# Performance work log

Hardware: AMD Instinct MI355X
Metric: run time of the kernel (lower is better)

## Reference

```python
import jax, jax.numpy as jnp
import numpy as np

D_ENC = 512
D_DEC = 512
JOINT = 512
VOCAB = 1024


def setup_inputs() -> dict:
    key = jax.random.key(0)
    ks = jax.random.split(key, 7)
    B, T, U = 4, 256, 64
    s_enc = 1.0 / np.sqrt(D_ENC)
    s_dec = 1.0 / np.sqrt(D_DEC)
    s_out = 1.0 / np.sqrt(JOINT)
    return {
        "encoder_out": jax.random.normal(ks[0], (B, T, 1, D_ENC), dtype=jnp.float32),
        "decoder_out": jax.random.normal(ks[1], (B, 1, U, D_DEC), dtype=jnp.float32),
        # torch.nn.Linear stores weight as (out, in); uniform(-1/sqrt(in), 1/sqrt(in))
        "W_enc": jax.random.uniform(ks[2], (JOINT, D_ENC), jnp.float32, -s_enc, s_enc),
        "b_enc": jax.random.uniform(ks[3], (JOINT,), jnp.float32, -s_enc, s_enc),
        "W_dec": jax.random.uniform(ks[4], (JOINT, D_DEC), jnp.float32, -s_dec, s_dec),
        "W_out": jax.random.uniform(ks[5], (VOCAB, JOINT), jnp.float32, -s_out, s_out),
        "b_out": jax.random.uniform(ks[6], (VOCAB,), jnp.float32, -s_out, s_out),
    }


def reference(encoder_out, decoder_out, W_enc, b_enc, W_dec, W_out, b_out):
    # Project each side in its small shape first (B,T,1,J) and (B,1,U,J),
    # then broadcast-add over (T,U), tanh, output GEMM -> (B,T,U,V).
    enc = jnp.einsum("btud,jd->btuj", encoder_out, W_enc) + b_enc  # (B,T,1,J)
    dec = jnp.einsum("btud,jd->btuj", decoder_out, W_dec)          # (B,1,U,J)
    h = jnp.tanh(enc + dec)                                        # (B,T,U,J)
    return jnp.einsum("btuj,vj->btuv", h, W_out) + b_out           # (B,T,U,V)
```

## Files before the change

kernel.cpp:

```cpp
#include <hip/hip_runtime.h>
#include <hip/hip_bf16.h>


typedef __attribute__((ext_vector_type(8))) short short8;
typedef __attribute__((ext_vector_type(4))) float f32x4;
typedef __attribute__((ext_vector_type(16))) float f32x16;

#define SZ0 524288
#define SZ1 131072
#define SZ2 262144
#define SZ3 512
#define SZ4 262144
#define SZ5 524288
#define SZ6 1024
#define CU0 0
#define CU1 524288
#define CU2 655360
#define CU3 917504
#define CU4 918016
#define CU5 1180160
#define CU6 1704448
#define CTOT 1705472

__global__ void detect_kernel(const void* p0, const void* p1, const void* p2,
                              const void* p3, const void* p4, const void* p5,
                              const void* p6, int* flags) {
  const void* ps[7] = {p0, p1, p2, p3, p4, p5, p6};
  const int sz[7] = {SZ0, SZ1, SZ2, SZ3, SZ4, SZ5, SZ6};
  const int w = threadIdx.x >> 6;
  const int l = threadIdx.x & 63;
  if (w >= 7) return;
  const unsigned short* u = (const unsigned short*)ps[w];
  const int lim = sz[w] < 1024 ? sz[w] : 1024;
  int bad = 0;
  for (int j = l; j < lim; j += 64) {
    const unsigned e = (u[j] >> 7) & 0xFFu;
    if (e >= 0x8Eu) bad = 1;
  }
  const unsigned long long b = __ballot(bad);
  if (l == 0) flags[w] = (b != 0ULL) ? 1 : 0;
}

__global__ __launch_bounds__(256) void convert_kernel(
    const void* p0, const void* p1, const void* p2, const void* p3,
    const void* p4, const void* p5, const void* p6,
    const int* __restrict__ flags, __hip_bfloat16* __restrict__ dst) {
  const int gid = blockIdx.x * 256 + threadIdx.x;
  if (gid >= CTOT) return;
  int t, local;
  const void* p;
  if (gid < CU1)      { t = 0; local = gid - CU0; p = p0; }
  else if (gid < CU2) { t = 1; local = gid - CU1; p = p1; }
  else if (gid < CU3) { t = 2; local = gid - CU2; p = p2; }
  else if (gid < CU4) { t = 3; local = gid - CU3; p = p3; }
  else if (gid < CU5) { t = 4; local = gid - CU4; p = p4; }
  else if (gid < CU6) { t = 5; local = gid - CU5; p = p5; }
  else                { t = 6; local = gid - CU6; p = p6; }
  __hip_bfloat16 v;
  if (flags[t])
    v = __float2bfloat16(((const float*)p)[local]);
  else
    v = ((const __hip_bfloat16*)p)[local];
  dst[gid] = v;
}

__device__ __forceinline__ void gemm_bt_body(
    const __hip_bfloat16* __restrict__ A, const __hip_bfloat16* __restrict__ Bw,
    const __hip_bfloat16* __restrict__ bias, float* __restrict__ C,
    int M, int N, int K, int bid,
    __hip_bfloat16* sA, __hip_bfloat16* sB) {
  const int tid = threadIdx.x;
  const int w = tid >> 6;
  const int l = tid & 63;
  const int ntiles = N >> 7;
  const int mt = bid / ntiles;
  const int nt = bid % ntiles;
  const int m0 = mt << 7;
  const int n0 = nt << 7;
  const int wm = (w >> 1) << 6;
  const int wn = (w & 1) << 6;
  const int r16 = l & 15;
  const int q = l >> 4;

  f32x4 acc[4][4] = {};

  const int srow_in = l >> 3;
  const int scol = (l & 7) << 3;

  for (int k0 = 0; k0 < K; k0 += 64) {
#pragma unroll
    for (int i = 0; i < 4; ++i) {
      const int c = (w << 2) + i;
      const int row = (c << 3) + srow_in;
      const __hip_bfloat16* gA = A + (size_t)(m0 + row) * K + k0 + scol;
      const __hip_bfloat16* gB = Bw + (size_t)(n0 + row) * K + k0 + scol;
      __builtin_amdgcn_global_load_lds(
          (const __attribute__((address_space(1))) void*)gA,
          (__attribute__((address_space(3))) void*)(sA + (c << 9) + (l << 3)),
          16, 0, 0);
      __builtin_amdgcn_global_load_lds(
          (const __attribute__((address_space(1))) void*)gB,
          (__attribute__((address_space(3))) void*)(sB + (c << 9) + (l << 3)),
          16, 0, 0);
    }
    __syncthreads();

#pragma unroll
    for (int kk = 0; kk < 2; ++kk) {
      const int kc = (kk << 5) + (q << 3);
      short8 af[4], bf[4];
#pragma unroll
      for (int mi = 0; mi < 4; ++mi)
        af[mi] = *(const short8*)(sA + (wm + (mi << 4) + r16) * 64 + kc);
#pragma unroll
      for (int ni = 0; ni < 4; ++ni)
        bf[ni] = *(const short8*)(sB + (wn + (ni << 4) + r16) * 64 + kc);
#pragma unroll
      for (int mi = 0; mi < 4; ++mi)
#pragma unroll
        for (int ni = 0; ni < 4; ++ni)
          acc[mi][ni] = __builtin_amdgcn_mfma_f32_16x16x32_bf16(
              af[mi], bf[ni], acc[mi][ni], 0, 0, 0);
    }
    __syncthreads();
  }

#pragma unroll
  for (int ni = 0; ni < 4; ++ni) {
    const int col = n0 + wn + (ni << 4) + r16;
    const float bc = bias ? __bfloat162float(bias[col]) : 0.0f;
#pragma unroll
    for (int mi = 0; mi < 4; ++mi) {
      const int rowb = m0 + wm + (mi << 4) + (q << 2);
#pragma unroll
      for (int i = 0; i < 4; ++i)
        C[(size_t)(rowb + i) * N + col] = acc[mi][ni][i] + bc;
    }
  }
}

__global__ __launch_bounds__(256) void proj_kernel(
    const __hip_bfloat16* __restrict__ enc, const __hip_bfloat16* __restrict__ Wenc,
    const __hip_bfloat16* __restrict__ benc,
    const __hip_bfloat16* __restrict__ dec, const __hip_bfloat16* __restrict__ Wdec,
    float* __restrict__ Pe, float* __restrict__ Pd) {
  __shared__ __align__(16) __hip_bfloat16 sA[128 * 64];
  __shared__ __align__(16) __hip_bfloat16 sB[128 * 64];
  if (blockIdx.x < 32)
    gemm_bt_body(enc, Wenc, benc, Pe, 1024, 512, 512, blockIdx.x, sA, sB);
  else
    gemm_bt_body(dec, Wdec, nullptr, Pd, 256, 512, 512, blockIdx.x - 32, sA, sB);
}

__global__ __launch_bounds__(512, 2) void gemm_joint(
    const float* __restrict__ Pe, const float* __restrict__ Pd,
    const __hip_bfloat16* __restrict__ Bw,
    const __hip_bfloat16* __restrict__ bias, float* __restrict__ out) {
  __shared__ __align__(16) __hip_bfloat16 sH[64 * 512];
  __shared__ __align__(16) __hip_bfloat16 sB[2 * 16384];

  const int t = threadIdx.x;
  const int w = t >> 6;
  const int l = t & 63;
  const int l31 = l & 31;
  const int q2 = l >> 5;
  const int m0 = blockIdx.x << 6;

  auto stage = [&](int ks, int bufbit) {
#pragma unroll
    for (int h = 0; h < 4; ++h) {
      const int n = (w << 7) + (h << 5) + (l >> 1);
      const __hip_bfloat16* src =
          Bw + (size_t)n * 512 + (ks << 4) + ((l & 1) << 3);
      __builtin_amdgcn_global_load_lds(
          (const __attribute__((address_space(1))) void*)src,
          (__attribute__((address_space(3))) void*)(
              sB + (bufbit << 14) + ((((w << 2) + h) << 9) + (l << 3))),
          16, 0, 0);
    }
  };

  stage(0, 0);

  {
    const int r = l;
    const int seg = w;
    const int d = ((blockIdx.x >> 8) << 6) | r;
    const float* pe = Pe + (size_t)blockIdx.x * 512 + (seg << 6);
    const float* pd = Pd + (size_t)d * 512 + (seg << 6);
#pragma unroll
    for (int i = 0; i < 8; ++i) {
      const int cc = (seg << 3) + i;
      const f32x4 a0 = *(const f32x4*)(pe + (i << 3));
      const f32x4 a1 = *(const f32x4*)(pe + (i << 3) + 4);
      const f32x4 b0 = *(const f32x4*)(pd + (i << 3));
      const f32x4 b1 = *(const f32x4*)(pd + (i << 3) + 4);
      short8 hv;
#pragma unroll
      for (int jj = 0; jj < 4; ++jj) {
        float s = a0[jj] + b0[jj];
        float tv = 1.0f - 2.0f / (__expf(2.0f * s) + 1.0f);
        __hip_bfloat16 hb = __float2bfloat16(tv);
        hv[jj] = *(const short*)&hb;
        s = a1[jj] + b1[jj];
        tv = 1.0f - 2.0f / (__expf(2.0f * s) + 1.0f);
        hb = __float2bfloat16(tv);
        hv[4 + jj] = *(const short*)&hb;
      }
      *(short8*)(sH + (r << 9) + ((cc ^ r) << 3)) = hv;
    }
  }
  __syncthreads();

  const int wn = w << 7;
  f32x16 acc[2][4] = {};

  for (int ks = 0; ks < 32; ++ks) {
    const int bufbit = ks & 1;
    if (ks < 31) {
      stage(ks + 1, bufbit ^ 1);
      asm volatile("s_waitcnt vmcnt(4)" ::: "memory");
    } else {
      asm volatile("s_waitcnt vmcnt(0)" ::: "memory");
    }
    __builtin_amdgcn_sched_barrier(0);
    __builtin_amdgcn_s_barrier();
    __builtin_amdgcn_sched_barrier(0);

    const int cb = (ks << 1) + q2;
    short8 af[2];
#pragma unroll
    for (int mi = 0; mi < 2; ++mi) {
      const int r = (mi << 5) + l31;
      af[mi] = *(const short8*)(sH + (r << 9) + ((cb ^ r) << 3));
    }
    short8 bf[4];
#pragma unroll
    for (int ni = 0; ni < 4; ++ni)
      bf[ni] = *(const short8*)(sB + (bufbit << 14) +
                                ((wn + (ni << 5) + l31) << 4) + (q2 << 3));
#pragma unroll
    for (int mi = 0; mi < 2; ++mi)
#pragma unroll
      for (int ni = 0; ni < 4; ++ni)
        acc[mi][ni] = __builtin_amdgcn_mfma_f32_32x32x16_bf16(
            af[mi], bf[ni], acc[mi][ni], 0, 0, 0);

    __builtin_amdgcn_sched_barrier(0);
    __builtin_amdgcn_s_barrier();
    __builtin_amdgcn_sched_barrier(0);
  }

#pragma unroll
  for (int ni = 0; ni < 4; ++ni) {
    const int col = wn + (ni << 5) + l31;
    const float bc = __bfloat162float(bias[col]);
#pragma unroll
    for (int mi = 0; mi < 2; ++mi) {
#pragma unroll
      for (int rr = 0; rr < 16; ++rr) {
        const int row = m0 + (mi << 5) + (rr & 3) + ((rr >> 2) << 3) + (q2 << 2);
        out[(size_t)row * 1024 + col] = acc[mi][ni][rr] + bc;
      }
    }
  }
}

extern "C" void kernel_launch(void* const* d_in, const int* in_sizes, int n_in,
                              void* d_out, int out_size, void* d_ws,
                              size_t ws_size, hipStream_t stream) {
  char* ws = (char*)d_ws;
  int* flags = (int*)ws;
  __hip_bfloat16* cp = (__hip_bfloat16*)(ws + 256);
  float* Pe = (float*)(ws + (4ull << 20));
  float* Pd = (float*)(ws + (6ull << 20));

  detect_kernel<<<dim3(1), dim3(512), 0, stream>>>(
      d_in[0], d_in[1], d_in[2], d_in[3], d_in[4], d_in[5], d_in[6], flags);
  convert_kernel<<<dim3((CTOT + 255) / 256), dim3(256), 0, stream>>>(
      d_in[0], d_in[1], d_in[2], d_in[3], d_in[4], d_in[5], d_in[6], flags, cp);

  const __hip_bfloat16* enc_c = cp + CU0;
  const __hip_bfloat16* dec_c = cp + CU1;
  const __hip_bfloat16* Wenc_c = cp + CU2;
  const __hip_bfloat16* benc_c = cp + CU3;
  const __hip_bfloat16* Wdec_c = cp + CU4;
  const __hip_bfloat16* Wout_c = cp + CU5;
  const __hip_bfloat16* bout_c = cp + CU6;

  proj_kernel<<<dim3(40), dim3(256), 0, stream>>>(enc_c, Wenc_c, benc_c,
                                                  dec_c, Wdec_c, Pe, Pd);
  gemm_joint<<<dim3(1024), dim3(512), 0, stream>>>(
      Pe, Pd, Wout_c, bout_c, (float*)d_out);
}
```

Measured before the change: 472.9 us.

## Retile joint GEMM to 128x256 blocks and compute tanh activations in-register

The joint GEMM changes from 64-row blocks covering all 1024 output columns to 128x256 tiles, doubling the grid. The tanh(enc+dec) activation tile is no longer staged in shared memory. Each warp reads Pe/Pd straight from global memory per k-step and builds its MFMA A fragments in registers, using a hardware reciprocal in place of a division. B tiles are 64-wide in k, XOR-swizzled, and double-buffered, and the reduced LDS allows a 4-blocks-per-CU occupancy hint. The cost is that tanh is recomputed for each of the 4 column blocks and the fp32 Pe/Pd reads from global move into the inner loop.

Result: faster. 445.5 us (-5.8%).

```diff
diff --git a/kernel.cpp b/kernel.cpp
--- a/kernel.cpp
+++ b/kernel.cpp
@@ -4,6 +4,7 @@
 
 typedef __attribute__((ext_vector_type(8))) short short8;
 typedef __attribute__((ext_vector_type(4))) float f32x4;
+typedef __attribute__((ext_vector_type(8))) float f32x8;
 typedef __attribute__((ext_vector_type(16))) float f32x16;
 
 #define SZ0 524288
@@ -152,73 +153,53 @@
     gemm_bt_body(dec, Wdec, nullptr, Pd, 256, 512, 512, blockIdx.x - 32, sA, sB);
 }
 
-__global__ __launch_bounds__(512, 2) void gemm_joint(
+__global__ __launch_bounds__(512, 4) void gemm_joint(
     const float* __restrict__ Pe, const float* __restrict__ Pd,
     const __hip_bfloat16* __restrict__ Bw,
     const __hip_bfloat16* __restrict__ bias, float* __restrict__ out) {
-  __shared__ __align__(16) __hip_bfloat16 sH[64 * 512];
-  __shared__ __align__(16) __hip_bfloat16 sB[2 * 16384];
+  __shared__ __align__(16) __hip_bfloat16 sB[2][256 * 64];
 
   const int t = threadIdx.x;
   const int w = t >> 6;
   const int l = t & 63;
   const int l31 = l & 31;
   const int q2 = l >> 5;
-  const int m0 = blockIdx.x << 6;
-
-  auto stage = [&](int ks, int bufbit) {
+  const int mb = blockIdx.x >> 2;
+  const int nb = blockIdx.x & 3;
+  const int m0 = mb << 7;
+  const int n0 = nb << 8;
+
+  auto stage = [&](int kt, int b) {
+    const int r_ = t >> 3;
+    const int c_ = t & 7;
 #pragma unroll
     for (int h = 0; h < 4; ++h) {
-      const int n = (w << 7) + (h << 5) + (l >> 1);
+      const int r = (h << 6) + r_;
       const __hip_bfloat16* src =
-          Bw + (size_t)n * 512 + (ks << 4) + ((l & 1) << 3);
+          Bw + (size_t)(n0 + r) * 512 + (kt << 6) + ((c_ ^ (r & 7)) << 3);
       __builtin_amdgcn_global_load_lds(
           (const __attribute__((address_space(1))) void*)src,
           (__attribute__((address_space(3))) void*)(
-              sB + (bufbit << 14) + ((((w << 2) + h) << 9) + (l << 3))),
+              &sB[b][0] + (h << 12) + (t << 3)),
           16, 0, 0);
     }
   };
 
+  const int wm = (w >> 1) << 5;
+  const int wn = (w & 1) << 7;
+
+  const float* peRow = Pe + (size_t)((m0 + wm) >> 6) * 512;
+  const int d = (((m0 >> 14) << 6) | ((wm + l31) & 63));
+  const float* pdRow = Pd + (size_t)d * 512;
+
+  f32x16 acc[4] = {};
+
   stage(0, 0);
 
-  {
-    const int r = l;
-    const int seg = w;
-    const int d = ((blockIdx.x >> 8) << 6) | r;
-    const float* pe = Pe + (size_t)blockIdx.x * 512 + (seg << 6);
-    const float* pd = Pd + (size_t)d * 512 + (seg << 6);
-#pragma unroll
-    for (int i = 0; i < 8; ++i) {
-      const int cc = (seg << 3) + i;
-      const f32x4 a0 = *(const f32x4*)(pe + (i << 3));
-      const f32x4 a1 = *(const f32x4*)(pe + (i << 3) + 4);
-      const f32x4 b0 = *(const f32x4*)(pd + (i << 3));
-      const f32x4 b1 = *(const f32x4*)(pd + (i << 3) + 4);
-      short8 hv;
-#pragma unroll
-      for (int jj = 0; jj < 4; ++jj) {
-        float s = a0[jj] + b0[jj];
-        float tv = 1.0f - 2.0f / (__expf(2.0f * s) + 1.0f);
-        __hip_bfloat16 hb = __float2bfloat16(tv);
-        hv[jj] = *(const short*)&hb;
-        s = a1[jj] + b1[jj];
-        tv = 1.0f - 2.0f / (__expf(2.0f * s) + 1.0f);
-        hb = __float2bfloat16(tv);
-        hv[4 + jj] = *(const short*)&hb;
-      }
-      *(short8*)(sH + (r << 9) + ((cc ^ r) << 3)) = hv;
-    }
-  }
-  __syncthreads();
-
-  const int wn = w << 7;
-  f32x16 acc[2][4] = {};
-
-  for (int ks = 0; ks < 32; ++ks) {
-    const int bufbit = ks & 1;
-    if (ks < 31) {
-      stage(ks + 1, bufbit ^ 1);
+  for (int kt = 0; kt < 8; ++kt) {
+    const int b = kt & 1;
+    if (kt < 7) {
+      stage(kt + 1, b ^ 1);
       asm volatile("s_waitcnt vmcnt(4)" ::: "memory");
     } else {
       asm volatile("s_waitcnt vmcnt(0)" ::: "memory");
@@ -227,24 +208,33 @@
     __builtin_amdgcn_s_barrier();
     __builtin_amdgcn_sched_barrier(0);
 
-    const int cb = (ks << 1) + q2;
-    short8 af[2];
-#pragma unroll
-    for (int mi = 0; mi < 2; ++mi) {
-      const int r = (mi << 5) + l31;
-      af[mi] = *(const short8*)(sH + (r << 9) + ((cb ^ r) << 3));
-    }
-    short8 bf[4];
-#pragma unroll
-    for (int ni = 0; ni < 4; ++ni)
-      bf[ni] = *(const short8*)(sB + (bufbit << 14) +
-                                ((wn + (ni << 5) + l31) << 4) + (q2 << 3));
-#pragma unroll
-    for (int mi = 0; mi < 2; ++mi)
+#pragma unroll
+    for (int j = 0; j < 4; ++j) {
+      const int kk = (kt << 6) + (j << 4) + (q2 << 3);
+      const f32x8 pe8 = *(const f32x8*)(peRow + kk);
+      const f32x8 pd8 = *(const f32x8*)(pdRow + kk);
+      short8 af;
+#pragma unroll
+      for (int x = 0; x < 8; ++x) {
+        const float s = pe8[x] + pd8[x];
+        const float u = __expf(2.0f * s);
+        const float tv = 1.0f - 2.0f * __builtin_amdgcn_rcpf(u + 1.0f);
+        const __hip_bfloat16 hb = __float2bfloat16(tv);
+        af[x] = *(const short*)&hb;
+      }
+      const int c = (j << 1) + q2;
+      short8 bf[4];
+#pragma unroll
+      for (int ni = 0; ni < 4; ++ni) {
+        const int row = wn + (ni << 5) + l31;
+        bf[ni] = *(const short8*)(&sB[b][0] + (row << 6) +
+                                  ((c ^ (row & 7)) << 3));
+      }
 #pragma unroll
       for (int ni = 0; ni < 4; ++ni)
-        acc[mi][ni] = __builtin_amdgcn_mfma_f32_32x32x16_bf16(
-            af[mi], bf[ni], acc[mi][ni], 0, 0, 0);
+        acc[ni] = __builtin_amdgcn_mfma_f32_32x32x16_bf16(
+            af, bf[ni], acc[ni], 0, 0, 0);
+    }
 
     __builtin_amdgcn_sched_barrier(0);
     __builtin_amdgcn_s_barrier();
@@ -253,15 +243,12 @@
 
 #pragma unroll
   for (int ni = 0; ni < 4; ++ni) {
-    const int col = wn + (ni << 5) + l31;
+    const int col = n0 + wn + (ni << 5) + l31;
     const float bc = __bfloat162float(bias[col]);
 #pragma unroll
-    for (int mi = 0; mi < 2; ++mi) {
-#pragma unroll
-      for (int rr = 0; rr < 16; ++rr) {
-        const int row = m0 + (mi << 5) + (rr & 3) + ((rr >> 2) << 3) + (q2 << 2);
-        out[(size_t)row * 1024 + col] = acc[mi][ni][rr] + bc;
-      }
+    for (int rr = 0; rr < 16; ++rr) {
+      const int row = m0 + wm + (rr & 3) + ((rr >> 2) << 3) + (q2 << 2);
+      out[(size_t)row * 1024 + col] = acc[ni][rr] + bc;
     }
   }
 }
@@ -290,6 +277,6 @@
 
   proj_kernel<<<dim3(40), dim3(256), 0, stream>>>(enc_c, Wenc_c, benc_c,
                                                   dec_c, Wdec_c, Pe, Pd);
-  gemm_joint<<<dim3(1024), dim3(512), 0, stream>>>(
+  gemm_joint<<<dim3(2048), dim3(512), 0, stream>>>(
       Pe, Pd, Wout_c, bout_c, (float*)d_out);
 }
```

## Pre-transpose W_out into k-chunk layout and stream H tile in quarters

Applied to the files above, without the earlier changes.

Extra blocks in the projection kernel write a copy of W_out reordered into k-chunk-major layout, so each stage of the joint GEMM loads one contiguous 32 KB slab with fully coalesced global_load_lds. The joint kernel now builds the tanh H tile in four 128-column quarters instead of all 512 columns at once. This shrinks the H LDS buffer from 64 KB to 16 KB, which may allow more resident blocks. The price is an extra syncthreads and a global reload of Pe/Pd every 8 k-steps, an added transpose pass over W_out, and an rcp-based tanh in place of a division.

New measurement: 423.4 us. -10.5%, faster.

```diff
diff --git a/kernel.cpp b/kernel.cpp
--- a/kernel.cpp
+++ b/kernel.cpp
@@ -4,6 +4,7 @@
 
 typedef __attribute__((ext_vector_type(8))) short short8;
 typedef __attribute__((ext_vector_type(4))) float f32x4;
+typedef __attribute__((ext_vector_type(8))) float f32x8;
 typedef __attribute__((ext_vector_type(16))) float f32x16;
 
 #define SZ0 524288
@@ -143,21 +144,33 @@
     const __hip_bfloat16* __restrict__ enc, const __hip_bfloat16* __restrict__ Wenc,
     const __hip_bfloat16* __restrict__ benc,
     const __hip_bfloat16* __restrict__ dec, const __hip_bfloat16* __restrict__ Wdec,
+    const __hip_bfloat16* __restrict__ Wout, __hip_bfloat16* __restrict__ WT,
     float* __restrict__ Pe, float* __restrict__ Pd) {
   __shared__ __align__(16) __hip_bfloat16 sA[128 * 64];
   __shared__ __align__(16) __hip_bfloat16 sB[128 * 64];
-  if (blockIdx.x < 32)
+  if (blockIdx.x < 32) {
     gemm_bt_body(enc, Wenc, benc, Pe, 1024, 512, 512, blockIdx.x, sA, sB);
-  else
+  } else if (blockIdx.x < 40) {
     gemm_bt_body(dec, Wdec, nullptr, Pd, 256, 512, 512, blockIdx.x - 32, sA, sB);
+  } else {
+    const int bid = blockIdx.x - 40;
+#pragma unroll
+    for (int i = 0; i < 32; ++i) {
+      const int cid = (bid << 13) + (i << 8) + threadIdx.x;
+      const int n = cid >> 6;
+      const int c = cid & 63;
+      *(short8*)(WT + (((size_t)c << 10) + n) * 8) =
+          *(const short8*)(Wout + (size_t)n * 512 + (c << 3));
+    }
+  }
 }
 
 __global__ __launch_bounds__(512, 2) void gemm_joint(
     const float* __restrict__ Pe, const float* __restrict__ Pd,
-    const __hip_bfloat16* __restrict__ Bw,
+    const __hip_bfloat16* __restrict__ WT,
     const __hip_bfloat16* __restrict__ bias, float* __restrict__ out) {
-  __shared__ __align__(16) __hip_bfloat16 sH[64 * 512];
-  __shared__ __align__(16) __hip_bfloat16 sB[2 * 16384];
+  __shared__ __align__(16) __hip_bfloat16 sH[16 * 64 * 8];
+  __shared__ __align__(16) __hip_bfloat16 sB[2][2 * 1024 * 8];
 
   const int t = threadIdx.x;
   const int w = t >> 6;
@@ -165,60 +178,54 @@
   const int l31 = l & 31;
   const int q2 = l >> 5;
   const int m0 = blockIdx.x << 6;
-
-  auto stage = [&](int ks, int bufbit) {
+  const int wn = w << 7;
+
+  auto stage = [&](int ks, int b) {
+    const __hip_bfloat16* src = WT + ((size_t)ks << 14);
 #pragma unroll
     for (int h = 0; h < 4; ++h) {
-      const int n = (w << 7) + (h << 5) + (l >> 1);
-      const __hip_bfloat16* src =
-          Bw + (size_t)n * 512 + (ks << 4) + ((l & 1) << 3);
+      const int slot = (h << 9) + t;
       __builtin_amdgcn_global_load_lds(
-          (const __attribute__((address_space(1))) void*)src,
-          (__attribute__((address_space(3))) void*)(
-              sB + (bufbit << 14) + ((((w << 2) + h) << 9) + (l << 3))),
+          (const __attribute__((address_space(1))) void*)(src + ((size_t)slot << 3)),
+          (__attribute__((address_space(3))) void*)(&sB[b][0] + (slot << 3)),
           16, 0, 0);
     }
   };
 
+  auto fillH = [&](int q) {
+    const float* peB = Pe + (size_t)blockIdx.x * 512 + (q << 7);
+    const int dbase = (blockIdx.x >> 8) << 6;
+#pragma unroll
+    for (int s2 = 0; s2 < 2; ++s2) {
+      const int s = (s2 << 9) + t;
+      const int r = s & 63;
+      const int cq = s >> 6;
+      const f32x8 a = *(const f32x8*)(peB + (cq << 3));
+      const f32x8 bv = *(const f32x8*)(Pd + (size_t)(dbase | r) * 512 +
+                                       (q << 7) + (cq << 3));
+      short8 hv;
+#pragma unroll
+      for (int x = 0; x < 8; ++x) {
+        const float sv = a[x] + bv[x];
+        const float u = __expf(2.0f * sv);
+        const float tv = 1.0f - 2.0f * __builtin_amdgcn_rcpf(u + 1.0f);
+        const __hip_bfloat16 hb = __float2bfloat16(tv);
+        hv[x] = *(const short*)&hb;
+      }
+      *(short8*)(sH + ((size_t)((cq << 6) + r) << 3)) = hv;
+    }
+  };
+
   stage(0, 0);
-
-  {
-    const int r = l;
-    const int seg = w;
-    const int d = ((blockIdx.x >> 8) << 6) | r;
-    const float* pe = Pe + (size_t)blockIdx.x * 512 + (seg << 6);
-    const float* pd = Pd + (size_t)d * 512 + (seg << 6);
-#pragma unroll
-    for (int i = 0; i < 8; ++i) {
-      const int cc = (seg << 3) + i;
-      const f32x4 a0 = *(const f32x4*)(pe + (i << 3));
-      const f32x4 a1 = *(const f32x4*)(pe + (i << 3) + 4);
-      const f32x4 b0 = *(const f32x4*)(pd + (i << 3));
-      const f32x4 b1 = *(const f32x4*)(pd + (i << 3) + 4);
-      short8 hv;
-#pragma unroll
-      for (int jj = 0; jj < 4; ++jj) {
-        float s = a0[jj] + b0[jj];
-        float tv = 1.0f - 2.0f / (__expf(2.0f * s) + 1.0f);
-        __hip_bfloat16 hb = __float2bfloat16(tv);
-        hv[jj] = *(const short*)&hb;
-        s = a1[jj] + b1[jj];
-        tv = 1.0f - 2.0f / (__expf(2.0f * s) + 1.0f);
-        hb = __float2bfloat16(tv);
-        hv[4 + jj] = *(const short*)&hb;
-      }
-      *(short8*)(sH + (r << 9) + ((cc ^ r) << 3)) = hv;
-    }
-  }
+  fillH(0);
   __syncthreads();
 
-  const int wn = w << 7;
   f32x16 acc[2][4] = {};
 
   for (int ks = 0; ks < 32; ++ks) {
-    const int bufbit = ks & 1;
+    const int b = ks & 1;
     if (ks < 31) {
-      stage(ks + 1, bufbit ^ 1);
+      stage(ks + 1, b ^ 1);
       asm volatile("s_waitcnt vmcnt(4)" ::: "memory");
     } else {
       asm volatile("s_waitcnt vmcnt(0)" ::: "memory");
@@ -227,18 +234,16 @@
     __builtin_amdgcn_s_barrier();
     __builtin_amdgcn_sched_barrier(0);
 
-    const int cb = (ks << 1) + q2;
+    const int cq = ((ks & 7) << 1) + q2;
     short8 af[2];
 #pragma unroll
-    for (int mi = 0; mi < 2; ++mi) {
-      const int r = (mi << 5) + l31;
-      af[mi] = *(const short8*)(sH + (r << 9) + ((cb ^ r) << 3));
-    }
+    for (int mi = 0; mi < 2; ++mi)
+      af[mi] = *(const short8*)(sH + (((cq << 6) + (mi << 5) + l31) << 3));
     short8 bf[4];
 #pragma unroll
     for (int ni = 0; ni < 4; ++ni)
-      bf[ni] = *(const short8*)(sB + (bufbit << 14) +
-                                ((wn + (ni << 5) + l31) << 4) + (q2 << 3));
+      bf[ni] = *(const short8*)(&sB[b][0] +
+                                (((q2 << 10) + wn + (ni << 5) + l31) << 3));
 #pragma unroll
     for (int mi = 0; mi < 2; ++mi)
 #pragma unroll
@@ -249,6 +254,11 @@
     __builtin_amdgcn_sched_barrier(0);
     __builtin_amdgcn_s_barrier();
     __builtin_amdgcn_sched_barrier(0);
+
+    if ((ks & 7) == 7 && ks < 31) {
+      fillH((ks + 1) >> 3);
+      __syncthreads();
+    }
   }
 
 #pragma unroll
@@ -274,6 +284,7 @@
   __hip_bfloat16* cp = (__hip_bfloat16*)(ws + 256);
   float* Pe = (float*)(ws + (4ull << 20));
   float* Pd = (float*)(ws + (6ull << 20));
+  __hip_bfloat16* WT = (__hip_bfloat16*)(ws + (8ull << 20));
 
   detect_kernel<<<dim3(1), dim3(512), 0, stream>>>(
       d_in[0], d_in[1], d_in[2], d_in[3], d_in[4], d_in[5], d_in[6], flags);
@@ -288,8 +299,8 @@
   const __hip_bfloat16* Wout_c = cp + CU5;
   const __hip_bfloat16* bout_c = cp + CU6;
 
-  proj_kernel<<<dim3(40), dim3(256), 0, stream>>>(enc_c, Wenc_c, benc_c,
-                                                  dec_c, Wdec_c, Pe, Pd);
+  proj_kernel<<<dim3(48), dim3(256), 0, stream>>>(
+      enc_c, Wenc_c, benc_c, dec_c, Wdec_c, Wout_c, WT, Pe, Pd);
   gemm_joint<<<dim3(1024), dim3(512), 0, stream>>>(
-      Pe, Pd, Wout_c, bout_c, (float*)d_out);
-}
+      Pe, Pd, WT, bout_c, (float*)d_out);
+}
```
